# Optimization experiments

Measured on AMD Instinct MI355X. Metric: run time of the kernel, lower is better.

## Reference

```python
import jax, jax.numpy as jnp
import numpy as np

B, T, E, H, D = 2, 2048, 1024, 16, 64  # D = attention_dim // num_heads

def setup_inputs() -> dict:
    key = jax.random.key(0)
    k1, k2, k3, k4 = jax.random.split(key, 4)
    scale = 1.0 / np.sqrt(E)  # ~ torch Linear init scale
    embedded = jax.random.normal(k1, (B, T, E), dtype=jnp.float32)
    Wq = jax.random.normal(k2, (H, D, E), dtype=jnp.float32) * scale
    Wk = jax.random.normal(k3, (H, D, E), dtype=jnp.float32) * scale
    Wv = jax.random.normal(k4, (H, D, E), dtype=jnp.float32) * scale
    return {"embedded": embedded, "Wq": Wq, "Wk": Wk, "Wv": Wv}

def reference(embedded, Wq, Wk, Wv):
    # Batched multi-head projection (original loops per head; same math).
    q = jnp.einsum('bte,hde->bhtd', embedded, Wq)
    k = jnp.einsum('bte,hde->bhtd', embedded, Wk)
    v = jnp.einsum('bte,hde->bhtd', embedded, Wv)
    scores = jnp.einsum('bhtd,bhsd->bhts', q, k) / jnp.sqrt(jnp.float32(D))
    causal = jnp.tril(jnp.ones((T, T), dtype=bool))  # [T,T]
    scores = jnp.where(causal, scores, -jnp.inf)
    attn = jax.nn.softmax(scores, axis=-1)
    out = jnp.einsum('bhts,bhsd->bhtd', attn, v)
    # concat heads on last dim: [B,T,H*D]
    return out.transpose(0, 2, 1, 3).reshape(B, T, H * D)
```

## Files before the change

### kernel.cpp

```cpp
#include <hip/hip_runtime.h>
#include <hip/hip_bf16.h>
#include <stdint.h>

typedef __bf16 bf16_t;
typedef __bf16 bf16x4 __attribute__((ext_vector_type(4)));
typedef __bf16 bf16x8 __attribute__((ext_vector_type(8)));
typedef float  f32x4  __attribute__((ext_vector_type(4)));

#define QK_SCALE 0.1803368801111204f

__device__ __forceinline__ void gload_lds16(const void* g, void* l) {
    __builtin_amdgcn_global_load_lds(
        (__attribute__((address_space(1))) unsigned int*)(uintptr_t)g,
        (__attribute__((address_space(3))) unsigned int*)(uint32_t)(uintptr_t)l,
        16, 0, 0);
}

__global__ __launch_bounds__(256) void convert_kernel(
    const float* __restrict__ emb, const float* __restrict__ wq,
    const float* __restrict__ wk,  const float* __restrict__ wv,
    bf16_t* __restrict__ embb, bf16_t* __restrict__ wcat)
{
    size_t base = ((size_t)blockIdx.x * 256 + threadIdx.x) * 8;
    const float* src;
    bf16_t* dst;
    if (base < (size_t)4194304) { src = emb + base; dst = embb + base; }
    else {
        size_t r = base - 4194304;
        int wsel = (int)(r >> 20);
        size_t off = r & 1048575;
        src = (wsel == 0 ? wq : (wsel == 1 ? wk : wv)) + off;
        dst = wcat + r;
    }
    float4 a  = *(const float4*)src;
    float4 c2 = *(const float4*)(src + 4);
    bf16x8 o;
    o[0]=(bf16_t)a.x;  o[1]=(bf16_t)a.y;  o[2]=(bf16_t)a.z;  o[3]=(bf16_t)a.w;
    o[4]=(bf16_t)c2.x; o[5]=(bf16_t)c2.y; o[6]=(bf16_t)c2.z; o[7]=(bf16_t)c2.w;
    *(bf16x8*)dst = o;
}

__global__ __launch_bounds__(256, 3) void proj_kernel(
    const bf16_t* __restrict__ A, const bf16_t* __restrict__ Wc,
    bf16_t* __restrict__ qo, bf16_t* __restrict__ ko, bf16_t* __restrict__ vto)
{
    __shared__ __align__(128) char smem[49152];

    const int tid  = threadIdx.x;
    const int w    = tid >> 6, lane = tid & 63;
    const int wr   = w >> 1,  wc2  = w & 1;
    const int g    = lane >> 4, c = lane & 15;
    const int bm   = blockIdx.x & 31, bn = blockIdx.x >> 5;
    const int m0   = bm * 128, n0 = bn * 128;

    f32x4 acc[4][4] = {};

    const int arow = lane >> 2;
    const int acol = (((lane & 3) ^ ((lane >> 3) & 3))) * 8;

    #define PROJ_STAGE(buf, kt)                                                        \
        do {                                                                           \
            char* As_ = smem + (buf) * 16384;                                          \
            char* Bs_ = As_ + 8192;                                                    \
            _Pragma("unroll")                                                          \
            for (int p = 0; p < 2; ++p) {                                              \
                gload_lds16(A  + (size_t)(m0 + p*64 + w*16 + arow) * 1024 + (kt)*32 + acol, \
                            As_ + (p*64 + w*16) * 64);                                 \
                gload_lds16(Wc + (size_t)(n0 + p*64 + w*16 + arow) * 1024 + (kt)*32 + acol, \
                            Bs_ + (p*64 + w*16) * 64);                                 \
            }                                                                          \
        } while (0)

    PROJ_STAGE(0, 0);
    PROJ_STAGE(1, 1);
    int cur = 0;
    for (int kt = 0; kt < 32; ++kt) {
        if (kt == 31) asm volatile("s_waitcnt vmcnt(0)" ::: "memory");
        else          asm volatile("s_waitcnt vmcnt(4)" ::: "memory");
        __builtin_amdgcn_s_barrier();
        asm volatile("" ::: "memory");
        if (kt + 2 < 32) {
            int b2 = cur + 2; if (b2 >= 3) b2 -= 3;
            PROJ_STAGE(b2, kt + 2);
        }
        const char* As = smem + cur * 16384;
        const char* Bs = As + 8192;
        const int sw = (c >> 1) & 3;
        bf16x8 af[4], bf[4];
        #pragma unroll
        for (int i = 0; i < 4; ++i) {
            af[i] = *(const bf16x8*)(As + (wr*64  + i*16 + c) * 64 + ((g ^ sw) << 4));
            bf[i] = *(const bf16x8*)(Bs + (wc2*64 + i*16 + c) * 64 + ((g ^ sw) << 4));
        }
        __builtin_amdgcn_s_setprio(1);
        #pragma unroll
        for (int i = 0; i < 4; ++i)
            #pragma unroll
            for (int j = 0; j < 4; ++j)
                acc[i][j] = __builtin_amdgcn_mfma_f32_16x16x32_bf16(af[i], bf[j], acc[i][j], 0, 0, 0);
        __builtin_amdgcn_s_setprio(0);
        cur = (cur == 2) ? 0 : cur + 1;
    }
    __syncthreads();

    const int b  = m0 >> 11;
    const int t0 = m0 & 2047;

    if (n0 < 2048) {
        bf16_t* dst = (n0 < 1024) ? qo : ko;
        const int nl0 = n0 & 1023;
        #pragma unroll
        for (int i = 0; i < 4; ++i)
            #pragma unroll
            for (int j = 0; j < 4; ++j) {
                int dl = wc2*64 + j*16 + c;
                #pragma unroll
                for (int e = 0; e < 4; ++e) {
                    int tl = wr*64 + i*16 + g*4 + e;
                    *(bf16_t*)(smem + ((tl*256 + dl*2) ^ ((tl & 7) << 4))) = (bf16_t)acc[i][j][e];
                }
            }
        __syncthreads();
        #pragma unroll
        for (int it = 0; it < 8; ++it) {
            int chunk = it * 256 + tid;
            int tl = chunk >> 4;
            int ce = (chunk & 15) * 8;
            bf16x8 val = *(const bf16x8*)(smem + ((tl*256 + ce*2) ^ ((tl & 7) << 4)));
            int nn = nl0 + ce;
            int hh = nn >> 6, dd = nn & 63;
            *(bf16x8*)(dst + ((size_t)(b*16 + hh) * 2048 + (t0 + tl)) * 64 + dd) = val;
        }
    } else {
        #pragma unroll
        for (int i = 0; i < 4; ++i)
            #pragma unroll
            for (int j = 0; j < 4; ++j) {
                int dl = wc2*64 + j*16 + c;
                #pragma unroll
                for (int e = 0; e < 4; ++e) {
                    int tl = wr*64 + i*16 + g*4 + e;
                    *(bf16_t*)(smem + ((dl*256 + tl*2) ^ ((dl & 7) << 4))) = (bf16_t)acc[i][j][e];
                }
            }
        __syncthreads();
        const int nvbase = n0 - 2048;
        #pragma unroll
        for (int it = 0; it < 8; ++it) {
            int chunk = it * 256 + tid;
            int dl = chunk >> 4;
            int tl = (chunk & 15) * 8;
            int B64 = tl >> 6;
            int r   = tl & 63;
            int t_a = B64*64 + ((r >> 3) & 1) * 32 + (r >> 4) * 4;
            bf16x4 lo = *(const bf16x4*)(smem + ((dl*256 + t_a*2)      ^ ((dl & 7) << 4)));
            bf16x4 hi = *(const bf16x4*)(smem + ((dl*256 + (t_a+16)*2) ^ ((dl & 7) << 4)));
            bf16x8 val = __builtin_shufflevector(lo, hi, 0, 1, 2, 3, 4, 5, 6, 7);
            int nv = nvbase + dl;
            int hh = nv >> 6, dd = nv & 63;
            *(bf16x8*)(vto + (size_t)((b*16 + hh)*64 + dd) * 2048 + t0 + tl) = val;
        }
    }
    #undef PROJ_STAGE
}

__global__ __launch_bounds__(512, 4) void attn_kernel(
    const bf16_t* __restrict__ qg, const bf16_t* __restrict__ kg,
    const bf16_t* __restrict__ vtg, float* __restrict__ out)
{
    __shared__ __align__(128) char smem[49152];

    const int tid = threadIdx.x;
    const int w = tid >> 6, lane = tid & 63;
    const int g = lane >> 4, c = lane & 15;
    const int id = blockIdx.x;
    const int j = id >> 5;
    const int qt = (j < 8) ? (15 - j) : (j - 8);
    const int bh = id & 31;
    const int b = bh >> 4, h = bh & 15;

    const bf16_t* qbase = qg  + (size_t)bh * 2048 * 64;
    const bf16_t* kbase = kg  + (size_t)bh * 2048 * 64;
    const bf16_t* vbase = vtg + (size_t)bh * 64 * 2048;
    float* obase = out + (size_t)b * 2048 * 1024 + h * 64;

    const int srow = lane >> 3;
    const int scol = ((lane & 7) ^ srow) * 8;

    const int q0 = qt * 128;
    const int nt = 2 * qt + 2;

    bf16x8 qf[2];
    #pragma unroll
    for (int kf = 0; kf < 2; ++kf) {
        bf16x8 v = *(const bf16x8*)(qbase + (size_t)(q0 + w*16 + c) * 64 + kf*32 + g*8);
        #pragma unroll
        for (int e = 0; e < 8; ++e) qf[kf][e] = (bf16_t)((float)v[e] * QK_SCALE);
    }

    f32x4 oacc[4] = {};
    float mrun = -INFINITY, lrun = 0.0f;

    #define ATTN_STAGE(buf, kt)                                                        \
        do {                                                                           \
            char* Kb_ = smem + (buf) * 16384;                                          \
            gload_lds16(kbase + (size_t)((kt)*64 + w*8 + srow) * 64 + scol,            \
                        Kb_ + w*1024);                                                 \
            gload_lds16(vbase + (size_t)(w*8 + srow) * 2048 + (kt)*64 + scol,          \
                        Kb_ + 8192 + w*1024);                                          \
        } while (0)

    ATTN_STAGE(0, 0);
    ATTN_STAGE(1, 1);
    int cur = 0;

    for (int kt = 0; kt < nt; ++kt) {
        if (kt == nt - 1) asm volatile("s_waitcnt vmcnt(0)" ::: "memory");
        else              asm volatile("s_waitcnt vmcnt(2)" ::: "memory");
        __builtin_amdgcn_s_barrier();
        asm volatile("" ::: "memory");
        if (kt + 2 < nt) {
            int b2 = cur + 2; if (b2 >= 3) b2 -= 3;
            ATTN_STAGE(b2, kt + 2);
        }
        const char* Ks = smem + cur * 16384;
        const char* Vs = Ks + 8192;

        f32x4 sacc[4];
        __builtin_amdgcn_s_setprio(1);
        #pragma unroll
        for (int ni = 0; ni < 4; ++ni) {
            int krow = ni*16 + c;
            bf16x8 k0 = *(const bf16x8*)(Ks + krow*128 + ((     g*16) ^ ((c & 7) << 4)));
            bf16x8 k1 = *(const bf16x8*)(Ks + krow*128 + ((64 + g*16) ^ ((c & 7) << 4)));
            f32x4 s0 = {0.f, 0.f, 0.f, 0.f};
            s0 = __builtin_amdgcn_mfma_f32_16x16x32_bf16(k0, qf[0], s0, 0, 0, 0);
            s0 = __builtin_amdgcn_mfma_f32_16x16x32_bf16(k1, qf[1], s0, 0, 0, 0);
            sacc[ni] = s0;
        }
        __builtin_amdgcn_s_setprio(0);

        if (kt >= nt - 2) {
            const int qloc = w*16 + c;
            const int koff = (kt - (nt - 2)) * 64;
            #pragma unroll
            for (int ni = 0; ni < 4; ++ni)
                #pragma unroll
                for (int e = 0; e < 4; ++e)
                    if (koff + ni*16 + g*4 + e > qloc) sacc[ni][e] = -INFINITY;
        }

        float pmax;
        {
            float t0_ = fmaxf(fmaxf(sacc[0][0], sacc[0][1]), sacc[0][2]);
            float t1_ = fmaxf(fmaxf(sacc[0][3], sacc[1][0]), sacc[1][1]);
            float t2_ = fmaxf(fmaxf(sacc[1][2], sacc[1][3]), sacc[2][0]);
            float t3_ = fmaxf(fmaxf(sacc[2][1], sacc[2][2]), sacc[2][3]);
            float t4_ = fmaxf(fmaxf(sacc[3][0], sacc[3][1]), sacc[3][2]);
            float u_  = fmaxf(fmaxf(t0_, t1_), t2_);
            float v_  = fmaxf(fmaxf(t3_, t4_), sacc[3][3]);
            pmax = fmaxf(u_, v_);
            pmax = fmaxf(pmax, __shfl_xor(pmax, 16));
            pmax = fmaxf(pmax, __shfl_xor(pmax, 32));
        }

        if (__any(pmax > mrun + 8.0f)) {
            float mnew = fmaxf(mrun, pmax);
            float sc = exp2f(mrun - mnew);
            float s0_ = __shfl(sc, g*4 + 0);
            float s1_ = __shfl(sc, g*4 + 1);
            float s2_ = __shfl(sc, g*4 + 2);
            float s3_ = __shfl(sc, g*4 + 3);
            #pragma unroll
            for (int db = 0; db < 4; ++db) {
                oacc[db][0] *= s0_; oacc[db][1] *= s1_;
                oacc[db][2] *= s2_; oacc[db][3] *= s3_;
            }
            lrun *= sc;
            mrun = mnew;
        }

        float psum = 0.f;
        bf16x8 palo, pahi;
        #pragma unroll
        for (int ni = 0; ni < 4; ++ni)
            #pragma unroll
            for (int e = 0; e < 4; ++e) {
                float pv = exp2f(sacc[ni][e] - mrun);
                psum += pv;
                if (ni < 2) palo[(ni & 1)*4 + e] = (bf16_t)pv;
                else        pahi[(ni & 1)*4 + e] = (bf16_t)pv;
            }

        __builtin_amdgcn_s_setprio(1);
        #pragma unroll
        for (int db = 0; db < 4; ++db) {
            int vrow = db*16 + c;
            bf16x8 vlo = *(const bf16x8*)(Vs + vrow*128 + ((g*32     ) ^ ((c & 7) << 4)));
            bf16x8 vhi = *(const bf16x8*)(Vs + vrow*128 + ((g*32 + 16) ^ ((c & 7) << 4)));
            oacc[db] = __builtin_amdgcn_mfma_f32_16x16x32_bf16(palo, vlo, oacc[db], 0, 0, 0);
            oacc[db] = __builtin_amdgcn_mfma_f32_16x16x32_bf16(pahi, vhi, oacc[db], 0, 0, 0);
        }
        __builtin_amdgcn_s_setprio(0);

        psum += __shfl_xor(psum, 16);
        psum += __shfl_xor(psum, 32);
        lrun += psum;

        cur = (cur == 2) ? 0 : cur + 1;
    }

    float inv[4];
    #pragma unroll
    for (int e = 0; e < 4; ++e) inv[e] = 1.0f / __shfl(lrun, g*4 + e);
    #pragma unroll
    for (int e = 0; e < 4; ++e) {
        size_t trow = (size_t)(q0 + w*16 + g*4 + e);
        #pragma unroll
        for (int db = 0; db < 4; ++db)
            obase[trow * 1024 + db*16 + c] = oacc[db][e] * inv[e];
    }
    #undef ATTN_STAGE
}

extern "C" void kernel_launch(void* const* d_in, const int* in_sizes, int n_in,
                              void* d_out, int out_size, void* d_ws, size_t ws_size,
                              hipStream_t stream) {
    const float* emb = (const float*)d_in[0];
    const float* wq  = (const float*)d_in[1];
    const float* wk  = (const float*)d_in[2];
    const float* wv  = (const float*)d_in[3];
    float* out = (float*)d_out;

    char* ws = (char*)d_ws;
    bf16_t* embb = (bf16_t*)ws;
    bf16_t* wcat = (bf16_t*)(ws + (size_t) 8*1024*1024);
    bf16_t* qb   = (bf16_t*)(ws + (size_t)14*1024*1024);
    bf16_t* kb   = (bf16_t*)(ws + (size_t)22*1024*1024);
    bf16_t* vtb  = (bf16_t*)(ws + (size_t)30*1024*1024);

    convert_kernel<<<3584, 256, 0, stream>>>(emb, wq, wk, wv, embb, wcat);
    proj_kernel<<<768, 256, 0, stream>>>(embb, wcat, qb, kb, vtb);
    attn_kernel<<<512, 512, 0, stream>>>(qb, kb, vtb, out);
}
```

Before: 151.3 us.

## Shrink attention blocks to 64 query rows with new tile-to-block schedule

The attention kernel now uses 256-thread blocks that each handle 64 query rows, launched as 1024 blocks instead of 512 blocks of 128 rows. Block ids map to (batch-head, query tile) through an interleaved, zig-zag ordering meant to balance causal work across CUs and group heads for L2 reuse. Each warp now loads twice as many K/V rows per stage. The row-sum shuffle reduction moves out of the loop to the end, and only the final tile needs causal masking. Finer blocks should reduce load imbalance and tail effects, at the cost of more K/V reloads per query row and different occupancy.

```diff
diff --git a/kernel.cpp b/kernel.cpp
--- a/kernel.cpp
+++ b/kernel.cpp
@@ -164,7 +164,7 @@
     #undef PROJ_STAGE
 }
 
-__global__ __launch_bounds__(512, 4) void attn_kernel(
+__global__ __launch_bounds__(256, 3) void attn_kernel(
     const bf16_t* __restrict__ qg, const bf16_t* __restrict__ kg,
     const bf16_t* __restrict__ vtg, float* __restrict__ out)
 {
@@ -174,9 +174,11 @@
     const int w = tid >> 6, lane = tid & 63;
     const int g = lane >> 4, c = lane & 15;
     const int id = blockIdx.x;
-    const int j = id >> 5;
-    const int qt = (j < 8) ? (15 - j) : (j - 8);
-    const int bh = id & 31;
+    const int x  = id & 7;
+    const int r  = id >> 3;
+    const int bh = x * 4 + (r & 3);
+    const int sr = r >> 2;
+    const int s  = (sr & 24) | (((sr >> 3) & 1) ? (7 - (sr & 7)) : (sr & 7));
     const int b = bh >> 4, h = bh & 15;
 
     const bf16_t* qbase = qg  + (size_t)bh * 2048 * 64;
@@ -187,8 +189,8 @@
     const int srow = lane >> 3;
     const int scol = ((lane & 7) ^ srow) * 8;
 
-    const int q0 = qt * 128;
-    const int nt = 2 * qt + 2;
+    const int nt = 32 - s;
+    const int q0 = (nt - 1) * 64;
 
     bf16x8 qf[2];
     #pragma unroll
@@ -201,22 +203,25 @@
     f32x4 oacc[4] = {};
     float mrun = -INFINITY, lrun = 0.0f;
 
-    #define ATTN_STAGE(buf, kt)                                                        \
-        do {                                                                           \
-            char* Kb_ = smem + (buf) * 16384;                                          \
-            gload_lds16(kbase + (size_t)((kt)*64 + w*8 + srow) * 64 + scol,            \
-                        Kb_ + w*1024);                                                 \
-            gload_lds16(vbase + (size_t)(w*8 + srow) * 2048 + (kt)*64 + scol,          \
-                        Kb_ + 8192 + w*1024);                                          \
+    #define ATTN_STAGE(buf, kt)                                                          \
+        do {                                                                             \
+            char* Kb_ = smem + (buf) * 16384;                                            \
+            _Pragma("unroll")                                                            \
+            for (int jj = 0; jj < 2; ++jj) {                                             \
+                gload_lds16(kbase + (size_t)((kt)*64 + w*16 + jj*8 + srow) * 64 + scol,  \
+                            Kb_ + (w*16 + jj*8) * 128);                                  \
+                gload_lds16(vbase + (size_t)(w*16 + jj*8 + srow) * 2048 + (kt)*64 + scol,\
+                            Kb_ + 8192 + (w*16 + jj*8) * 128);                           \
+            }                                                                            \
         } while (0)
 
     ATTN_STAGE(0, 0);
-    ATTN_STAGE(1, 1);
+    if (nt > 1) ATTN_STAGE(1, 1);
     int cur = 0;
 
     for (int kt = 0; kt < nt; ++kt) {
         if (kt == nt - 1) asm volatile("s_waitcnt vmcnt(0)" ::: "memory");
-        else              asm volatile("s_waitcnt vmcnt(2)" ::: "memory");
+        else              asm volatile("s_waitcnt vmcnt(4)" ::: "memory");
         __builtin_amdgcn_s_barrier();
         asm volatile("" ::: "memory");
         if (kt + 2 < nt) {
@@ -240,14 +245,13 @@
         }
         __builtin_amdgcn_s_setprio(0);
 
-        if (kt >= nt - 2) {
+        if (kt == nt - 1) {
             const int qloc = w*16 + c;
-            const int koff = (kt - (nt - 2)) * 64;
             #pragma unroll
             for (int ni = 0; ni < 4; ++ni)
                 #pragma unroll
                 for (int e = 0; e < 4; ++e)
-                    if (koff + ni*16 + g*4 + e > qloc) sacc[ni][e] = -INFINITY;
+                    if (ni*16 + g*4 + e > qloc) sacc[ni][e] = -INFINITY;
         }
 
         float pmax;
@@ -291,6 +295,7 @@
                 if (ni < 2) palo[(ni & 1)*4 + e] = (bf16_t)pv;
                 else        pahi[(ni & 1)*4 + e] = (bf16_t)pv;
             }
+        lrun += psum;
 
         __builtin_amdgcn_s_setprio(1);
         #pragma unroll
@@ -303,13 +308,11 @@
         }
         __builtin_amdgcn_s_setprio(0);
 
-        psum += __shfl_xor(psum, 16);
-        psum += __shfl_xor(psum, 32);
-        lrun += psum;
-
         cur = (cur == 2) ? 0 : cur + 1;
     }
 
+    lrun += __shfl_xor(lrun, 16);
+    lrun += __shfl_xor(lrun, 32);
     float inv[4];
     #pragma unroll
     for (int e = 0; e < 4; ++e) inv[e] = 1.0f / __shfl(lrun, g*4 + e);
@@ -341,5 +344,5 @@
 
     convert_kernel<<<3584, 256, 0, stream>>>(emb, wq, wk, wv, embb, wcat);
     proj_kernel<<<768, 256, 0, stream>>>(embb, wcat, qb, kb, vtb);
-    attn_kernel<<<512, 512, 0, stream>>>(qb, kb, vtb, out);
-}
+    attn_kernel<<<1024, 256, 0, stream>>>(qb, kb, vtb, out);
+}
```

Result: no change. 150.9 us (-0.2%).
